# Kernel tuning notes

Hardware: AMD Instinct MI355X
Metric: run time of the kernel (lower is better)

The kernel has to match this reference:

```python
import jax, jax.numpy as jnp
import numpy as np

B, S, D, H, DFF = 2, 4096, 512, 8, 2048
DK = D // H
EPS = 1e-5


def layer_norm(x, g, b):
    mu = jnp.mean(x, axis=-1, keepdims=True)
    var = jnp.mean((x - mu) ** 2, axis=-1, keepdims=True)
    return (x - mu) * jax.lax.rsqrt(var + EPS) * g + b


def setup_inputs() -> dict:
    key = jax.random.key(0)
    ks = jax.random.split(key, 12)
    s = 1.0 / np.sqrt(D)
    return {
        "x": jax.random.normal(ks[0], (B, S, D), jnp.float32),
        "mask": jnp.ones((B, 1, 1, S), jnp.int32),
        "wq": jax.random.normal(ks[1], (D, D), jnp.float32) * s,
        "wk": jax.random.normal(ks[2], (D, D), jnp.float32) * s,
        "wv": jax.random.normal(ks[3], (D, D), jnp.float32) * s,
        "wo": jax.random.normal(ks[4], (D, D), jnp.float32) * s,
        "w1": jax.random.normal(ks[5], (D, DFF), jnp.float32) * s,
        "b1": jnp.zeros((DFF,), jnp.float32),
        "w2": jax.random.normal(ks[6], (DFF, D), jnp.float32) * (1.0 / np.sqrt(DFF)),
        "b2": jnp.zeros((D,), jnp.float32),
        "g1": jnp.ones((D,), jnp.float32),
        "be1": jnp.zeros((D,), jnp.float32),
        "g2": jnp.ones((D,), jnp.float32),
        "be2": jnp.zeros((D,), jnp.float32),
    }


def reference(x, mask, wq, wk, wv, wo, w1, b1, w2, b2, g1, be1, g2, be2):
    # projections -> [B, H, S, DK]
    def split_heads(t):
        return t.reshape(B, S, H, DK).transpose(0, 2, 1, 3)

    q = split_heads(x @ wq)
    k = split_heads(x @ wk)
    v = split_heads(x @ wv)

    scores = jnp.einsum("bhqd,bhkd->bhqk", q, k) / np.sqrt(DK)
    scores = jnp.where(mask == 0, -1e9, scores)
    attn = jax.nn.softmax(scores, axis=-1)  # dropout=0 (eval)
    ctx = jnp.einsum("bhqk,bhkd->bhqd", attn, v)
    ctx = ctx.transpose(0, 2, 1, 3).reshape(B, S, D)
    attn_out = ctx @ wo

    x1 = layer_norm(x + attn_out, g1, be1)
    ff = jax.nn.relu(x1 @ w1 + b1) @ w2 + b2
    return layer_norm(x1 + ff, g2, be2)
```

## Files before the change

kernel.cpp:

```cpp
#include <hip/hip_runtime.h>
#include <hip/hip_bf16.h>


typedef unsigned short u16;
typedef unsigned int u32;
typedef __attribute__((ext_vector_type(2))) u32 u32x2;
typedef __attribute__((ext_vector_type(4))) u16 u16x4;
typedef __attribute__((ext_vector_type(8))) u16 u16x8;
typedef __attribute__((ext_vector_type(2))) float f32x2;
typedef __attribute__((ext_vector_type(4))) float f32x4;
typedef __attribute__((ext_vector_type(16))) float f32x16;
typedef __attribute__((ext_vector_type(8))) short bf16x8;

#define CB 2
#define CS 4096
#define CD 512
#define CH 8
#define CDK 64
#define CDFF 2048
#define NXC ((size_t)CB * CS * CD)
#define NSP 2
#define BH (CB * CH)
#define BHS (BH * CS)

__device__ __forceinline__ float bf2f(u16 u) {
    union { u32 i; float f; } c;
    c.i = ((u32)u) << 16;
    return c.f;
}

__device__ __forceinline__ u16 f2bf(float f) {
    u32 x = __float_as_uint(f);
    u32 r = (x + 0x7fffu + ((x >> 16) & 1u)) >> 16;
    return (u16)r;
}

__device__ __forceinline__ u32 packbf2(float a, float b) {
    __hip_bfloat162 h = __float22bfloat162_rn(float2{a, b});
    union { __hip_bfloat162 h; u32 u; } c;
    c.h = h;
    return c.u;
}

__device__ __forceinline__ void dma16(const u16* g, u16* l) {
    __builtin_amdgcn_global_load_lds(
        (const __attribute__((address_space(1))) void*)g,
        (__attribute__((address_space(3))) void*)l, 16, 0, 0);
}

__global__ void detect_dtype(const u32* __restrict__ xw, int* __restrict__ flag) {
    __shared__ int red[256];
    int sane = 0;
    for (int i = threadIdx.x; i < 2048; i += 256) {
        u32 w = xw[i];
        u32 lo = w & 0xFFFFu;
        u32 e = (lo >> 7) & 0xFFu;
        if (lo == 0u || lo == 0x8000u || (e >= 96u && e <= 159u)) sane++;
    }
    red[threadIdx.x] = sane;
    __syncthreads();
    for (int s = 128; s > 0; s >>= 1) {
        if ((int)threadIdx.x < s) red[threadIdx.x] += red[threadIdx.x + s];
        __syncthreads();
    }
    if (threadIdx.x == 0) *flag = (red[0] >= 1843) ? 1 : 0;
}

__global__ __launch_bounds__(256) void convert_bf16(
    const void* __restrict__ src, u16* __restrict__ dst, int n,
    const int* __restrict__ flag)
{
    const bool isbf = (*flag != 0);
    const int n8 = n >> 3;
    int i = blockIdx.x * 256 + threadIdx.x;
    const int stride = gridDim.x * 256;
    if (isbf) {
        const u16x8* s = (const u16x8*)src;
        u16x8* d = (u16x8*)dst;
        for (; i < n8; i += stride) d[i] = s[i];
    } else {
        const f32x4* s = (const f32x4*)src;
        for (; i < n8; i += stride) {
            f32x4 a = s[2 * i];
            f32x4 b = s[2 * i + 1];
            u16x8 o;
#pragma unroll
            for (int e = 0; e < 4; e++) {
                o[e] = f2bf(a[e]);
                o[4 + e] = f2bf(b[e]);
            }
            *(u16x8*)&dst[(size_t)i * 8] = o;
        }
    }
    if (blockIdx.x == 0 && threadIdx.x == 0) {
        for (int r = n8 * 8; r < n; r++) {
            if (isbf) dst[r] = ((const u16*)src)[r];
            else dst[r] = f2bf(((const float*)src)[r]);
        }
    }
}

struct PrepArgs {
    const void* tsrc[6];
    u16* tdst[6];
    int R[6], Cc[6], nbx[6];
    int cum[7];
    const int* mask;
    unsigned long long* bits;
    const void* ssrc[6];
    u16* sdst[6];
    int sn[6];
};

__global__ __launch_bounds__(256) void prep_all(PrepArgs pa, const int* __restrict__ flag) {
    const int bid = blockIdx.x;
    const int tid = threadIdx.x;
    if (bid < pa.cum[6]) {
        __shared__ float t[32][33];
        int w = 0;
#pragma unroll
        for (int k = 1; k < 6; k++) w += (bid >= pa.cum[k]) ? 1 : 0;
        const int local = bid - pa.cum[w];
        const int nbx = pa.nbx[w];
        const int bx = local % nbx;
        const int by = local / nbx;
        const int R = pa.R[w];
        const int Cc = pa.Cc[w];
        const void* src = pa.tsrc[w];
        u16* dst = pa.tdst[w];
        const bool isbf = (*flag != 0);
        const int r0 = by * 32;
        const int c0 = bx * 32;
        const int col = tid & 31;
        const int row = tid >> 5;
#pragma unroll
        for (int it = 0; it < 4; it++) {
            int rr = row + it * 8;
            float v;
            if (isbf) v = bf2f(((const u16*)src)[(size_t)(r0 + rr) * Cc + c0 + col]);
            else v = ((const float*)src)[(size_t)(r0 + rr) * Cc + c0 + col];
            t[rr][col] = v;
        }
        __syncthreads();
#pragma unroll
        for (int it = 0; it < 4; it++) {
            int rr = row + it * 8;
            dst[(size_t)(c0 + rr) * R + r0 + col] = f2bf(t[col][rr]);
        }
    } else if (bid < pa.cum[6] + 32) {
        const int local = bid - pa.cum[6];
        int w = local * 4 + (tid >> 6);
        int lane = tid & 63;
        int b = w >> 6, t = w & 63;
        int val = pa.mask[b * CS + t * 64 + lane];
        unsigned long long bal = __ballot(val != 0);
        if (lane == 0) pa.bits[w] = bal;
    } else {
        const bool isbf = (*flag != 0);
        for (int t = 0; t < 6; t++) {
            for (int i = tid; i < pa.sn[t]; i += 256) {
                if (isbf) pa.sdst[t][i] = ((const u16*)pa.ssrc[t])[i];
                else pa.sdst[t][i] = f2bf(((const float*)pa.ssrc[t])[i]);
            }
        }
    }
}

#define F_SPLIT 1
#define F_BIAS  2
#define F_RELU  4

template <int FLAGS>
__global__ __launch_bounds__(512, 2) void gemm256(
    const u16* __restrict__ A, const u16* __restrict__ Bt,
    const u16* __restrict__ bias, u16* __restrict__ C,
    int M, int N, int K)
{
    __shared__ __align__(16) u16 POOL[65536 + 8 * 1536];

    const int tid = threadIdx.x;
    const int lane = tid & 63;
    const int wave = tid >> 6;
    const int lrow = lane & 15;
    const int quad = lane >> 4;
    const int rswg = lrow & 7;
    const int wm = wave >> 2;
    const int wn = wave & 3;
    const int m0 = blockIdx.y * 256;
    const int n0 = blockIdx.x * 256;

    const u16* Asrc[4];
    const u16* Bsrc[4];
#pragma unroll
    for (int r = 0; r < 4; r++) {
        const int idx = r * 512 + tid;
        const int row = idx >> 3;
        const int g = (idx & 7) ^ (row & 7);
        Asrc[r] = A + (size_t)(m0 + row) * K + g * 8;
        Bsrc[r] = Bt + (size_t)(n0 + row) * K + g * 8;
    }

#define STG256(BUF, K0)                                                      \
    {                                                                        \
        _Pragma("unroll")                                                    \
        for (int r = 0; r < 4; r++) {                                        \
            dma16(Asrc[r] + (K0), &POOL[(BUF) * 32768 + r * 4096 + wave * 512]); \
            dma16(Bsrc[r] + (K0), &POOL[(BUF) * 32768 + 16384 + r * 4096 + wave * 512]); \
        }                                                                    \
    }

    f32x4 acc[8][4];
#pragma unroll
    for (int mi = 0; mi < 8; mi++)
#pragma unroll
        for (int ni = 0; ni < 4; ni++) acc[mi][ni] = f32x4{0.f, 0.f, 0.f, 0.f};

    const int NT = K >> 6;
    STG256(0, 0)

    for (int j = 0; j < NT; j++) {
        asm volatile("s_waitcnt vmcnt(0)" ::: "memory");
        __builtin_amdgcn_sched_barrier(0);
        __builtin_amdgcn_s_barrier();
        __builtin_amdgcn_sched_barrier(0);
        if (j + 1 < NT) STG256((j + 1) & 1, (j + 1) * 64)

        const char* Ab = (const char*)&POOL[(j & 1) * 32768];
        const char* Bb = (const char*)&POOL[(j & 1) * 32768 + 16384];
#pragma unroll
        for (int ks = 0; ks < 2; ks++) {
            bf16x8 af[8], bfr[4];
#pragma unroll
            for (int mi = 0; mi < 8; mi++) {
                const int row = wm * 128 + mi * 16 + lrow;
                af[mi] = *(const bf16x8*)(Ab + row * 128 +
                                          (((ks * 4 + quad) ^ rswg) << 4));
            }
#pragma unroll
            for (int ni = 0; ni < 4; ni++) {
                const int row = wn * 64 + ni * 16 + lrow;
                bfr[ni] = *(const bf16x8*)(Bb + row * 128 +
                                           (((ks * 4 + quad) ^ rswg) << 4));
            }
#pragma unroll
            for (int mi = 0; mi < 8; mi++)
#pragma unroll
                for (int ni = 0; ni < 4; ni++)
                    acc[mi][ni] = __builtin_amdgcn_mfma_f32_16x16x32_bf16(
                        af[mi], bfr[ni], acc[mi][ni], 0, 0, 0);
        }
    }
#undef STG256

    u16* st = POOL + 65536 + wave * 1536;
    const int mbase = m0 + wm * 128;
    const int nbase = n0 + wn * 64;
    const int msub = mbase & 4095;
    const int bb = mbase >> 12;
    const bool vpath = (FLAGS & F_SPLIT) && ((nbase >> 9) == 2);

    if (vpath) {
        const int h = (nbase >> 6) & 7;
        u16* vdst = C + 2 * NXC + (((size_t)(bb * CH + h)) * CDK) * CS;
#pragma unroll
        for (int mi = 0; mi < 8; mi++) {
#pragma unroll
            for (int ni = 0; ni < 4; ni++)
#pragma unroll
                for (int r = 0; r < 4; r++)
                    st[(ni * 16 + lrow) * 24 + quad * 4 + r] = f2bf(acc[mi][ni][r]);
#pragma unroll
            for (int rr = 0; rr < 2; rr++) {
                const int idx = rr * 64 + lane;
                const int dk = idx >> 1;
                const int sch = idx & 1;
                u16x8 val = *(const u16x8*)&st[dk * 24 + sch * 8];
                *(u16x8*)&vdst[(size_t)dk * CS + msub + mi * 16 + sch * 8] = val;
            }
        }
    } else {
        float bv[4];
        if (FLAGS & F_BIAS) {
#pragma unroll
            for (int ni = 0; ni < 4; ni++) bv[ni] = bf2f(bias[nbase + ni * 16 + lrow]);
        }
        const int proj = nbase >> 9;
        const int h = (nbase >> 6) & 7;
        u16* qkdst = C + (size_t)proj * NXC + (((size_t)(bb * CH + h)) * CS) * CDK;
#pragma unroll
        for (int mi = 0; mi < 8; mi++) {
#pragma unroll
            for (int ni = 0; ni < 4; ni++)
#pragma unroll
                for (int r = 0; r < 4; r++) {
                    float val = acc[mi][ni][r];
                    if (FLAGS & F_BIAS) val += bv[ni];
                    if (FLAGS & F_RELU) val = fmaxf(val, 0.f);
                    st[(quad * 4 + r) * 68 + ni * 16 + lrow] = f2bf(val);
                }
#pragma unroll
            for (int rr = 0; rr < 2; rr++) {
                const int idx = rr * 64 + lane;
                const int row = idx >> 3;
                const int ch = idx & 7;
                u16x4 lo = *(const u16x4*)&st[row * 68 + ch * 8];
                u16x4 hi = *(const u16x4*)&st[row * 68 + ch * 8 + 4];
                u16x8 val;
#pragma unroll
                for (int e = 0; e < 4; e++) { val[e] = lo[e]; val[4 + e] = hi[e]; }
                u16* p;
                if (FLAGS & F_SPLIT)
                    p = qkdst + (size_t)(msub + mi * 16 + row) * CDK + ch * 8;
                else
                    p = C + (size_t)(mbase + mi * 16 + row) * N + nbase + ch * 8;
                *(u16x8*)p = val;
            }
        }
    }
}

template <int FLAGS, int PIPE>
__global__ __launch_bounds__(256, PIPE ? 1 : 3) void gemm_mfma(
    const u16* __restrict__ A, const u16* __restrict__ Bt,
    const u16* __restrict__ bias, u16* __restrict__ C,
    int M, int N, int K)
{
    constexpr int ABn = PIPE ? 12288 : 8192;
    __shared__ __align__(16) u16 POOL[2 * ABn + 4 * 1536];
    u16* ASb = POOL;
    u16* BSb = POOL + ABn;

    const int tid = threadIdx.x;
    const int lane = tid & 63;
    const int wave = tid >> 6;
    const int lrow = lane & 15;
    const int quad = lane >> 4;
    const int wm = wave & 1;
    const int wn = wave >> 1;
    const int m0 = blockIdx.y * 128;
    const int n0 = blockIdx.x * 128;

    f32x4 acc[4][4];
#pragma unroll
    for (int i = 0; i < 4; i++)
#pragma unroll
        for (int j = 0; j < 4; j++) acc[i][j] = f32x4{0.f, 0.f, 0.f, 0.f};

    if constexpr (PIPE) {
        const int idx0 = wave * 128 + lane;
        const int idx1 = idx0 + 64;
        const u16* Ap0 = A + (size_t)(m0 + (idx0 >> 2)) * K + (idx0 & 3) * 8;
        const u16* Ap1 = A + (size_t)(m0 + (idx1 >> 2)) * K + (idx1 & 3) * 8;
        const u16* Bp0 = Bt + (size_t)(n0 + (idx0 >> 2)) * K + (idx0 & 3) * 8;
        const u16* Bp1 = Bt + (size_t)(n0 + (idx1 >> 2)) * K + (idx1 & 3) * 8;
        const int NK = K >> 5;

#define PSTAGE(BOFF, KOFF)                                                   \
        {                                                                    \
            dma16(Ap0 + (KOFF), ASb + (BOFF) + wave * 1024);                 \
            dma16(Ap1 + (KOFF), ASb + (BOFF) + wave * 1024 + 512);           \
            dma16(Bp0 + (KOFF), BSb + (BOFF) + wave * 1024);                 \
            dma16(Bp1 + (KOFF), BSb + (BOFF) + wave * 1024 + 512);           \
        }
        PSTAGE(0, 0)
        PSTAGE(4096, 32)
        u32 bR = 0;
        for (int j = 0; j < NK; j++) {
            if (j < NK - 1) { asm volatile("s_waitcnt vmcnt(4)" ::: "memory"); }
            else            { asm volatile("s_waitcnt vmcnt(0)" ::: "memory"); }
            __builtin_amdgcn_sched_barrier(0);
            __builtin_amdgcn_s_barrier();
            __builtin_amdgcn_sched_barrier(0);
            if (j + 2 < NK) {
                u32 bS = bR + 8192;
                if (bS >= 12288) bS -= 12288;
                PSTAGE(bS, (j + 2) * 32)
            }
            bf16x8 af[4], bfr[4];
#pragma unroll
            for (int i = 0; i < 4; i++)
                af[i] = *(const bf16x8*)&ASb[bR + (wm * 64 + i * 16 + lrow) * 32 + quad * 8];
#pragma unroll
            for (int jj = 0; jj < 4; jj++)
                bfr[jj] = *(const bf16x8*)&BSb[bR + (wn * 64 + jj * 16 + lrow) * 32 + quad * 8];
#pragma unroll
            for (int i = 0; i < 4; i++)
#pragma unroll
                for (int jj = 0; jj < 4; jj++)
                    acc[i][jj] = __builtin_amdgcn_mfma_f32_16x16x32_bf16(
                        af[i], bfr[jj], acc[i][jj], 0, 0, 0);
            bR = (bR == 8192u) ? 0u : bR + 4096u;
        }
#undef PSTAGE
    } else {
        const int rswg = lrow & 7;
        const u16* Aps[4];
        const u16* Bps[4];
        u16* Adst[4];
        u16* Bdst[4];
#pragma unroll
        for (int r = 0; r < 4; r++) {
            const int idx = r * 256 + tid;
            const int row = idx >> 3;
            const int g = (idx & 7) ^ (row & 7);
            Aps[r] = A + (size_t)(m0 + row) * K + g * 8;
            Bps[r] = Bt + (size_t)(n0 + row) * K + g * 8;
            Adst[r] = &ASb[r * 2048 + wave * 512];
            Bdst[r] = &BSb[r * 2048 + wave * 512];
        }
        const char* As8 = (const char*)ASb;
        const char* Bs8 = (const char*)BSb;

        for (int k0 = 0; k0 < K; k0 += 64) {
            __syncthreads();
#pragma unroll
            for (int r = 0; r < 4; r++) {
                dma16(Aps[r] + k0, Adst[r]);
                dma16(Bps[r] + k0, Bdst[r]);
            }
            __syncthreads();

#pragma unroll
            for (int kk = 0; kk < 2; kk++) {
                bf16x8 af[4], bfr[4];
#pragma unroll
                for (int i = 0; i < 4; i++) {
                    const int row = wm * 64 + i * 16 + lrow;
                    af[i] = *(const bf16x8*)(As8 + row * 128 +
                                             (((kk * 4 + quad) ^ rswg) << 4));
                }
#pragma unroll
                for (int j = 0; j < 4; j++) {
                    const int row = wn * 64 + j * 16 + lrow;
                    bfr[j] = *(const bf16x8*)(Bs8 + row * 128 +
                                              (((kk * 4 + quad) ^ rswg) << 4));
                }
#pragma unroll
                for (int i = 0; i < 4; i++)
#pragma unroll
                    for (int j = 0; j < 4; j++)
                        acc[i][j] = __builtin_amdgcn_mfma_f32_16x16x32_bf16(
                            af[i], bfr[j], acc[i][j], 0, 0, 0);
            }
        }
    }

    u16* st = POOL + 2 * ABn + wave * 1536;
    const int mbase = m0 + wm * 64;
    const int nbase = n0 + wn * 64;
    const int msub = mbase & 4095;
    const int bb = mbase >> 12;
    const bool vpath = (FLAGS & F_SPLIT) && ((nbase >> 9) == 2);

    if (vpath) {
        const int h = (nbase >> 6) & 7;
        u16* vdst = C + 2 * NXC + (((size_t)(bb * CH + h)) * CDK) * CS;
#pragma unroll
        for (int i = 0; i < 4; i++) {
#pragma unroll
            for (int j = 0; j < 4; j++)
#pragma unroll
                for (int r = 0; r < 4; r++)
                    st[(j * 16 + lrow) * 24 + quad * 4 + r] = f2bf(acc[i][j][r]);
#pragma unroll
            for (int rr = 0; rr < 2; rr++) {
                const int idx = rr * 64 + lane;
                const int dk = idx >> 1;
                const int sch = idx & 1;
                u16x8 val = *(const u16x8*)&st[dk * 24 + sch * 8];
                *(u16x8*)&vdst[(size_t)dk * CS + msub + i * 16 + sch * 8] = val;
            }
        }
    } else {
        float bv[4];
        if (FLAGS & F_BIAS) {
#pragma unroll
            for (int j = 0; j < 4; j++) bv[j] = bf2f(bias[nbase + j * 16 + lrow]);
        }
        const int proj = nbase >> 9;
        const int h = (nbase >> 6) & 7;
        u16* qkdst = C + (size_t)proj * NXC + (((size_t)(bb * CH + h)) * CS) * CDK;
#pragma unroll
        for (int i = 0; i < 4; i++) {
#pragma unroll
            for (int j = 0; j < 4; j++)
#pragma unroll
                for (int r = 0; r < 4; r++) {
                    float val = acc[i][j][r];
                    if (FLAGS & F_BIAS) val += bv[j];
                    if (FLAGS & F_RELU) val = fmaxf(val, 0.f);
                    st[(quad * 4 + r) * 68 + j * 16 + lrow] = f2bf(val);
                }
#pragma unroll
            for (int rr = 0; rr < 2; rr++) {
                const int idx = rr * 64 + lane;
                const int row = idx >> 3;
                const int ch = idx & 7;
                u16x4 lo = *(const u16x4*)&st[row * 68 + ch * 8];
                u16x4 hi = *(const u16x4*)&st[row * 68 + ch * 8 + 4];
                u16x8 val;
#pragma unroll
                for (int e = 0; e < 4; e++) { val[e] = lo[e]; val[4 + e] = hi[e]; }
                u16* p;
                if (FLAGS & F_SPLIT)
                    p = qkdst + (size_t)(msub + i * 16 + row) * CDK + ch * 8;
                else
                    p = C + (size_t)(mbase + i * 16 + row) * N + nbase + ch * 8;
                *(u16x8*)p = val;
            }
        }
    }
}

__global__ __launch_bounds__(256, 4) void mfma_attn2(
    const u16* __restrict__ Qb, const u16* __restrict__ Kb,
    const u16* __restrict__ Vt, const unsigned long long* __restrict__ bits,
    u16* __restrict__ pOT, float* __restrict__ Ls)
{
    __shared__ u16 KB[3][4096];
    __shared__ u16 VB[2][4096];

    const int tid = threadIdx.x;
    const int lane = tid & 63;
    const int wave = tid >> 6;
    const int qcol = lane & 31;
    const int hf = lane >> 5;

    const int bh = blockIdx.y;
    const int b = bh >> 3;
    const int z = blockIdx.z;
    const int q0 = blockIdx.x * 128 + wave * 32;

    const float SC = 0.125f * 1.44269504088896340736f;

    bf16x8 bq[4];
    const u16* qp = Qb + ((size_t)bh * CS + q0 + qcol) * CDK + hf * 8;
#pragma unroll
    for (int c = 0; c < 4; c++) {
        bf16x8 raw = *(const bf16x8*)(qp + c * 16);
        union { u32 u[4]; bf16x8 v; } cv;
#pragma unroll
        for (int j = 0; j < 4; j++)
            cv.u[j] = packbf2(bf2f((u16)raw[2 * j]) * SC, bf2f((u16)raw[2 * j + 1]) * SC);
        bq[c] = cv.v;
    }

    f32x4 z4 = {0.f, 0.f, 0.f, 0.f};
    asm volatile("" : "+v"(z4));
    f32x16 zero16;
#pragma unroll
    for (int i = 0; i < 16; i++) zero16[i] = z4[i & 3];

    f32x16 ot[2];
#pragma unroll
    for (int dt = 0; dt < 2; dt++)
#pragma unroll
        for (int i = 0; i < 16; i++) ot[dt][i] = 0.f;
    float lh = 0.f;

    const u16* kbase = Kb + (size_t)bh * CS * CDK;
    const u16* vbase = Vt + (size_t)bh * CDK * CS;
    const unsigned long long* bp = bits + b * 64;

    const int t0 = z * (CS / NSP);
    const int t1 = t0 + (CS / NSP);

    const int rsw = qcol & 7;
    int koff[2][4];
#pragma unroll
    for (int rt = 0; rt < 2; rt++)
#pragma unroll
        for (int c = 0; c < 4; c++)
            koff[rt][c] = ((rt * 32 + qcol) * 64 + (((2 * c + hf) ^ rsw) * 8)) * 2;
    const char* kb0 = (const char*)&KB[0][0];
    const char* vb0 = (const char*)&VB[0][0];

    const int w2 = wave * 2;

#define STAGE_K(KOFFB, t)                                                    \
    {                                                                        \
        const u16* kb_ = kbase + (size_t)(t) * CDK;                          \
        _Pragma("unroll")                                                    \
        for (int n = 0; n < 2; n++) {                                        \
            int idx = (w2 + n) * 64 + lane;                                  \
            int row = idx >> 3;                                              \
            int g = (idx & 7) ^ (row & 7);                                   \
            dma16(kb_ + row * CDK + g * 8,                                   \
                  (u16*)((char*)&KB[0][0] + (KOFFB) + (w2 + n) * 1024));     \
        }                                                                    \
    }
#define STAGE_V(P, t)                                                        \
    {                                                                        \
        const u16* vb_ = vbase + (t);                                        \
        _Pragma("unroll")                                                    \
        for (int n = 0; n < 2; n++) {                                        \
            int idx = (w2 + n) * 64 + lane;                                  \
            int row = idx >> 3;                                              \
            int g = (idx & 7) ^ (row & 7);                                   \
            dma16(vb_ + (size_t)row * CS + g * 8,                            \
                  (u16*)((char*)&VB[0][0] + (P) * 8192 + (w2 + n) * 1024));  \
        }                                                                    \
    }

#define TBODY(KROFF, VOFF, BM, MASKED, MIDSYNC)                              \
    {                                                                        \
        f32x2 racc = {0.f, 0.f};                                             \
        _Pragma("unroll")                                                    \
        for (int mt = 0; mt < 2; mt++) {                                     \
            f32x16 s;                                                        \
            _Pragma("unroll")                                                \
            for (int c = 0; c < 4; c++) {                                    \
                bf16x8 ak = *(const bf16x8*)(kb0 + (KROFF) + koff[mt][c]);   \
                s = __builtin_amdgcn_mfma_f32_32x32x16_bf16(                 \
                    ak, bq[c], (c == 0) ? zero16 : s, 0, 0, 0);              \
            }                                                                \
            if (MASKED) {                                                    \
                const unsigned long long bm_ = (BM);                         \
                if (bm_ != ~0ull) {                                          \
                    _Pragma("unroll")                                        \
                    for (int i = 0; i < 16; i++) {                           \
                        const int key = (i & 3) + 8 * (i >> 2) + 4 * hf + 32 * mt; \
                        if (!((bm_ >> key) & 1ull)) s[i] = -1e30f;           \
                    }                                                        \
                }                                                            \
            }                                                                \
            u32 pk[8];                                                       \
            _Pragma("unroll")                                                \
            for (int g = 0; g < 4; g++) {                                    \
                float p0 = __builtin_amdgcn_exp2f(s[4 * g + 0]);             \
                float p1 = __builtin_amdgcn_exp2f(s[4 * g + 1]);             \
                float p2 = __builtin_amdgcn_exp2f(s[4 * g + 2]);             \
                float p3 = __builtin_amdgcn_exp2f(s[4 * g + 3]);             \
                racc += f32x2{p0, p1};                                       \
                racc += f32x2{p2, p3};                                       \
                pk[2 * g + 0] = packbf2(p0, p1);                             \
                pk[2 * g + 1] = packbf2(p2, p3);                             \
            }                                                                \
            if (mt == 0) { MIDSYNC }                                         \
            _Pragma("unroll")                                                \
            for (int cc = 0; cc < 2; cc++) {                                 \
                u32x2 r0 = __builtin_amdgcn_permlane32_swap(                 \
                    pk[4 * cc + 0], pk[4 * cc + 2], false, false);           \
                u32x2 r1 = __builtin_amdgcn_permlane32_swap(                 \
                    pk[4 * cc + 1], pk[4 * cc + 3], false, false);           \
                union { u32 u[4]; bf16x8 v; } pf;                            \
                pf.u[0] = r0.x;                                              \
                pf.u[1] = r1.x;                                              \
                pf.u[2] = r0.y;                                              \
                pf.u[3] = r1.y;                                              \
                const int c = 2 * mt + cc;                                   \
                _Pragma("unroll")                                            \
                for (int dt = 0; dt < 2; dt++) {                             \
                    bf16x8 av = *(const bf16x8*)(vb0 + (VOFF) + koff[dt][c]); \
                    ot[dt] = __builtin_amdgcn_mfma_f32_32x32x16_bf16(        \
                        av, pf.v, ot[dt], 0, 0, 0);                          \
                }                                                            \
            }                                                                \
        }                                                                    \
        lh += racc.x + racc.y;                                               \
    }

#define FTILE(P, TT, KR, KS, DOV, DOK, TOPASM, MIDASM)                       \
    {                                                                        \
        asm volatile(TOPASM ::: "memory");                                   \
        __builtin_amdgcn_sched_barrier(0);                                   \
        __builtin_amdgcn_s_barrier();                                        \
        __builtin_amdgcn_sched_barrier(0);                                   \
        if (DOV) STAGE_V((P) ^ 1, (TT) + 64);                                \
        if (DOK) STAGE_K((KS), (TT) + 128);                                  \
        TBODY((KR), (P) * 8192, 0ull, 0,                                     \
              asm volatile(MIDASM ::: "memory");                             \
              __builtin_amdgcn_sched_barrier(0);                             \
              __builtin_amdgcn_s_barrier();                                  \
              __builtin_amdgcn_sched_barrier(0);)                            \
    }

    unsigned long long am = ~0ull;
    const int tb0 = t0 >> 6;
    for (int i = 0; i < 32; i++) am &= bp[tb0 + i];
    const bool allones = (am == ~0ull);

    if (allones) {
        STAGE_K(0, t0);
        STAGE_V(0, t0);
        STAGE_K(8192, t0 + 64);

        u32 kr = 0;
        for (int m = 0; m < 15; m++) {
            const int t = t0 + m * 128;
            const u32 kr1 = (kr == 16384u) ? 0u : kr + 8192u;
            const u32 ks0 = (kr1 == 16384u) ? 0u : kr1 + 8192u;
            FTILE(0, t, kr, ks0, 1, 1,
                  "s_waitcnt vmcnt(4)", "s_waitcnt vmcnt(6)")
            FTILE(1, t + 64, kr1, kr, 1, 1,
                  "s_waitcnt vmcnt(4)", "s_waitcnt vmcnt(6)")
            kr = ks0;
        }
        {
            const int t = t0 + 30 * 64;
            const u32 kr1 = (kr == 16384u) ? 0u : kr + 8192u;
            FTILE(0, t, kr, 0, 1, 0,
                  "s_waitcnt vmcnt(4)", "s_waitcnt vmcnt(4)")
            FTILE(1, t + 64, kr1, 0, 0, 0,
                  "s_waitcnt vmcnt(2)", "s_waitcnt vmcnt(0)")
        }
    } else {
        STAGE_K(0, t0);
        STAGE_V(0, t0);
        __syncthreads();
        for (int t = t0; t < t1; t += 64) {
            const int p = (t >> 6) & 1;
            const u32 kro = (u32)p * 8192u;
            if (t + 64 < t1) {
                STAGE_V(p ^ 1, t + 64);
                STAGE_K((p ^ 1) * 8192, t + 64);
            }
            TBODY(kro, p * 8192, bp[t >> 6], 1, ;)
            __syncthreads();
        }
    }
#undef FTILE
#undef TBODY
#undef STAGE_V
#undef STAGE_K

    u32x2 rr = __builtin_amdgcn_permlane32_swap(
        __float_as_uint(lh), __float_as_uint(lh), false, false);
    const float l = lh + __uint_as_float(hf ? rr.x : rr.y);

    const int q_lin = bh * CS + q0 + qcol;
    if (hf == 0) Ls[z * BHS + q_lin] = l;
    const size_t pbase = ((size_t)(z * BH + bh) * CDK) * CS + q0 + qcol;
#pragma unroll
    for (int dt = 0; dt < 2; dt++)
#pragma unroll
        for (int i = 0; i < 16; i++) {
            const int dk = (i & 3) + 8 * (i >> 2) + 4 * hf + 32 * dt;
            pOT[pbase + (size_t)dk * CS] = f2bf(ot[dt][i]);
        }
}

__global__ __launch_bounds__(256) void attn_combine(
    const u16* __restrict__ pOT, const float* __restrict__ Ls,
    u16* __restrict__ ctx)
{
    __shared__ float linv[64];
    __shared__ u16 T[64][72];

    const int bh = blockIdx.y;
    const int s0 = blockIdx.x * 64;
    const int b = bh >> 3, h = bh & 7;
    const int tid = threadIdx.x;

    if (tid < 64) {
        float L = 0.f;
#pragma unroll
        for (int z = 0; z < NSP; z++) L += Ls[z * BHS + bh * CS + s0 + tid];
        linv[tid] = (L > 0.f) ? 1.f / L : 0.f;
    }
    __syncthreads();

    const int dk = tid >> 2;
    const int sc = (tid & 3) * 16;
    float acc[16] = {};
#pragma unroll
    for (int z = 0; z < NSP; z++) {
        const u16* p = pOT + ((size_t)(z * BH + bh) * CDK + dk) * CS + s0 + sc;
        u16x8 v0 = *(const u16x8*)p;
        u16x8 v1 = *(const u16x8*)(p + 8);
#pragma unroll
        for (int e = 0; e < 8; e++) {
            acc[e] += bf2f(v0[e]);
            acc[8 + e] += bf2f(v1[e]);
        }
    }
#pragma unroll
    for (int e = 0; e < 16; e++)
        T[sc + e][dk] = f2bf(acc[e] * linv[sc + e]);
    __syncthreads();

    const int sr = tid >> 2;
    const int dc = (tid & 3) * 16;
    u16x8 o0, o1;
#pragma unroll
    for (int e = 0; e < 8; e++) {
        o0[e] = T[sr][dc + e];
        o1[e] = T[sr][dc + 8 + e];
    }
    u16* cp = &ctx[((size_t)b * CS + s0 + sr) * CD + h * CDK + dc];
    *(u16x8*)cp = o0;
    *(u16x8*)(cp + 8) = o1;
}

__global__ __launch_bounds__(256) void ln_kernel(
    const u16* __restrict__ xa, const u16* __restrict__ xb,
    const u16* __restrict__ g, const u16* __restrict__ be,
    u16* __restrict__ outb, float* __restrict__ outf,
    const int* __restrict__ flag)
{
    const int lane = threadIdx.x & 63;
    const int wave = threadIdx.x >> 6;
    const size_t row = (size_t)blockIdx.x * 4 + wave;
    const int c0 = lane * 8;

    u16x8 av = *(const u16x8*)(xa + row * CD + c0);
    u16x8 bv = *(const u16x8*)(xb + row * CD + c0);

    float v[8];
    float s1 = 0.f, s2 = 0.f;
#pragma unroll
    for (int e = 0; e < 8; e++) {
        v[e] = bf2f(av[e]) + bf2f(bv[e]);
        s1 += v[e];
        s2 += v[e] * v[e];
    }
#pragma unroll
    for (int off = 32; off > 0; off >>= 1) {
        s1 += __shfl_xor(s1, off, 64);
        s2 += __shfl_xor(s2, off, 64);
    }
    const float mu = s1 * (1.f / CD);
    const float var = fmaxf(s2 * (1.f / CD) - mu * mu, 0.f);
    const float r = rsqrtf(var + 1e-5f);

    u16x8 gv = *(const u16x8*)(g + c0);
    u16x8 ev = *(const u16x8*)(be + c0);
    float res[8];
#pragma unroll
    for (int e = 0; e < 8; e++)
        res[e] = (v[e] - mu) * r * bf2f(gv[e]) + bf2f(ev[e]);

    const int flg = *flag;
    const bool f32out = (outf != nullptr) && (flg == 0);
    if (f32out) {
        float4 o0 = make_float4(res[0], res[1], res[2], res[3]);
        float4 o1 = make_float4(res[4], res[5], res[6], res[7]);
        *(float4*)(outf + row * CD + c0) = o0;
        *(float4*)(outf + row * CD + c0 + 4) = o1;
    } else {
        u16x8 ov;
#pragma unroll
        for (int e = 0; e < 8; e++) ov[e] = f2bf(res[e]);
        *(u16x8*)(outb + row * CD + c0) = ov;
    }
}


extern "C" void kernel_launch(void* const* d_in, const int* in_sizes, int n_in,
                              void* d_out, int out_size, void* d_ws, size_t ws_size,
                              hipStream_t stream)
{
    const void* x_raw   = d_in[0];
    const int*  mask    = (const int*)d_in[1];
    const void* wq_raw  = d_in[2];
    const void* wk_raw  = d_in[3];
    const void* wv_raw  = d_in[4];
    const void* wo_raw  = d_in[5];
    const void* w1_raw  = d_in[6];
    const void* b1_raw  = d_in[7];
    const void* w2_raw  = d_in[8];
    const void* b2_raw  = d_in[9];
    const void* g1_raw  = d_in[10];
    const void* be1_raw = d_in[11];
    const void* g2_raw  = d_in[12];
    const void* be2_raw = d_in[13];

    const size_t NX = NXC;
    const size_t WSZ = (size_t)CD * CD;
    const size_t W1SZ = (size_t)CD * CDFF;

    u16* ws = (u16*)d_ws;
    int* flag = (int*)d_ws;
    unsigned long long* bits = (unsigned long long*)(ws + 512);
    u16* base = ws + 1024;
    u16* xc  = base;
    u16* q   = base + 1 * NX;
    u16* k   = base + 2 * NX;
    u16* v   = base + 3 * NX;
    u16* ctx = base + 4 * NX;
    u16* att = base + 5 * NX;
    u16* x1  = base + 6 * NX;
    u16* ffo = base + 7 * NX;
    u16* ffh = base + 8 * NX;
    u16* wt  = base + 12 * NX;
    u16* wqkvT = wt;
    u16* woT = wqkvT + 3 * WSZ;
    u16* w1T = woT + WSZ;
    u16* w2T = w1T + W1SZ;
    u16* b1c = w2T + W1SZ;
    u16* b2c = b1c + CDFF;
    u16* g1c = b2c + CD;
    u16* be1c = g1c + CD;
    u16* g2c = be1c + CD;
    u16* be2c = g2c + CD;
    u16* wend = be2c + CD;

    const size_t need = (size_t)(wend - ws) * sizeof(u16);
    if (ws_size < need) return;
    (void)k;

    u16* pOT = ffh;
    float* Ls = (float*)att;

    detect_dtype<<<1, 256, 0, stream>>>((const u32*)x_raw, flag);

    convert_bf16<<<1024, 256, 0, stream>>>(x_raw, xc, (int)NX, flag);

    PrepArgs pa;
    pa.tsrc[0] = wq_raw; pa.tdst[0] = wqkvT;           pa.R[0] = CD;   pa.Cc[0] = CD;
    pa.tsrc[1] = wk_raw; pa.tdst[1] = wqkvT + WSZ;     pa.R[1] = CD;   pa.Cc[1] = CD;
    pa.tsrc[2] = wv_raw; pa.tdst[2] = wqkvT + 2 * WSZ; pa.R[2] = CD;   pa.Cc[2] = CD;
    pa.tsrc[3] = wo_raw; pa.tdst[3] = woT;             pa.R[3] = CD;   pa.Cc[3] = CD;
    pa.tsrc[4] = w1_raw; pa.tdst[4] = w1T;             pa.R[4] = CD;   pa.Cc[4] = CDFF;
    pa.tsrc[5] = w2_raw; pa.tdst[5] = w2T;             pa.R[5] = CDFF; pa.Cc[5] = CD;
    int cum = 0;
    for (int w = 0; w < 6; w++) {
        pa.nbx[w] = pa.Cc[w] / 32;
        pa.cum[w] = cum;
        cum += (pa.Cc[w] / 32) * (pa.R[w] / 32);
    }
    pa.cum[6] = cum;
    pa.mask = mask;
    pa.bits = bits;
    pa.ssrc[0] = b1_raw;  pa.sdst[0] = b1c;  pa.sn[0] = CDFF;
    pa.ssrc[1] = b2_raw;  pa.sdst[1] = b2c;  pa.sn[1] = CD;
    pa.ssrc[2] = g1_raw;  pa.sdst[2] = g1c;  pa.sn[2] = CD;
    pa.ssrc[3] = be1_raw; pa.sdst[3] = be1c; pa.sn[3] = CD;
    pa.ssrc[4] = g2_raw;  pa.sdst[4] = g2c;  pa.sn[4] = CD;
    pa.ssrc[5] = be2_raw; pa.sdst[5] = be2c; pa.sn[5] = CD;
    prep_all<<<cum + 32 + 1, 256, 0, stream>>>(pa, flag);

    const int M = CB * CS;

    gemm256<F_SPLIT><<<dim3(1536 / 256, M / 256), 512, 0, stream>>>(
        xc, wqkvT, nullptr, q, M, 1536, CD);

    mfma_attn2<<<dim3(CS / 128, BH, NSP), 256, 0, stream>>>(q, k, v, bits, pOT, Ls);
    attn_combine<<<dim3(CS / 64, BH), 256, 0, stream>>>(pOT, Ls, ctx);

    gemm_mfma<0, 1><<<dim3(CD / 128, M / 128), 256, 0, stream>>>(
        ctx, woT, nullptr, att, M, CD, CD);

    ln_kernel<<<dim3(M / 4), 256, 0, stream>>>(xc, att, g1c, be1c, x1, nullptr, flag);

    gemm256<F_BIAS | F_RELU><<<dim3(CDFF / 256, M / 256), 512, 0, stream>>>(
        x1, w1T, b1c, ffh, M, CDFF, CD);
    gemm_mfma<F_BIAS, 1><<<dim3(CD / 128, M / 128), 256, 0, stream>>>(
        ffh, w2T, b2c, ffo, M, CD, CDFF);

    ln_kernel<<<dim3(M / 4), 256, 0, stream>>>(x1, ffo, g2c, be2c,
                                               (u16*)d_out, (float*)d_out, flag);
}
```

Baseline: 300.9 us.

## Deepen GEMM prefetch pipeline, remap attention blocks per XCD, prioritize MFMA

The PIPE GEMM goes from a 3-slot to a 6-slot LDS ring buffer, keeping five stages of global-to-LDS DMA in flight with an explicitly drained tail to hide more memory latency. The attention launch becomes a flat 1D grid whose block index is decoded so each XCD handles contiguous (bh, split) pairs, aiming for better L2 reuse of K/V. s_setprio is raised around the attention MFMA sequences to favour issue of matrix work. The larger GEMM LDS footprint may reduce occupancy, though that kernel already runs one block per SM.

```diff
diff --git a/kernel.cpp b/kernel.cpp
--- a/kernel.cpp
+++ b/kernel.cpp
@@ -325,7 +325,7 @@
     const u16* __restrict__ bias, u16* __restrict__ C,
     int M, int N, int K)
 {
-    constexpr int ABn = PIPE ? 12288 : 8192;
+    constexpr int ABn = PIPE ? 24576 : 8192;
     __shared__ __align__(16) u16 POOL[2 * ABn + 4 * 1536];
     u16* ASb = POOL;
     u16* BSb = POOL + ABn;
@@ -362,35 +362,48 @@
             dma16(Bp0 + (KOFF), BSb + (BOFF) + wave * 1024);                 \
             dma16(Bp1 + (KOFF), BSb + (BOFF) + wave * 1024 + 512);           \
         }
+#define PITER(VMASM, DOS, JS)                                                \
+        {                                                                    \
+            asm volatile(VMASM ::: "memory");                                \
+            __builtin_amdgcn_sched_barrier(0);                               \
+            __builtin_amdgcn_s_barrier();                                    \
+            __builtin_amdgcn_sched_barrier(0);                               \
+            if (DOS) {                                                       \
+                u32 bS = bR + 20480u;                                        \
+                if (bS >= 24576u) bS -= 24576u;                              \
+                PSTAGE(bS, ((JS) + 5) * 32)                                  \
+            }                                                                \
+            bf16x8 af[4], bfr[4];                                            \
+            _Pragma("unroll")                                                \
+            for (int i = 0; i < 4; i++)                                      \
+                af[i] = *(const bf16x8*)&ASb[bR + (wm * 64 + i * 16 + lrow) * 32 + quad * 8]; \
+            _Pragma("unroll")                                                \
+            for (int jj = 0; jj < 4; jj++)                                   \
+                bfr[jj] = *(const bf16x8*)&BSb[bR + (wn * 64 + jj * 16 + lrow) * 32 + quad * 8]; \
+            _Pragma("unroll")                                                \
+            for (int i = 0; i < 4; i++)                                      \
+                _Pragma("unroll")                                            \
+                for (int jj = 0; jj < 4; jj++)                               \
+                    acc[i][jj] = __builtin_amdgcn_mfma_f32_16x16x32_bf16(    \
+                        af[i], bfr[jj], acc[i][jj], 0, 0, 0);                \
+            bR += 4096u;                                                     \
+            if (bR == 24576u) bR = 0u;                                       \
+        }
+
         PSTAGE(0, 0)
         PSTAGE(4096, 32)
+        PSTAGE(8192, 64)
+        PSTAGE(12288, 96)
+        PSTAGE(16384, 128)
         u32 bR = 0;
-        for (int j = 0; j < NK; j++) {
-            if (j < NK - 1) { asm volatile("s_waitcnt vmcnt(4)" ::: "memory"); }
-            else            { asm volatile("s_waitcnt vmcnt(0)" ::: "memory"); }
-            __builtin_amdgcn_sched_barrier(0);
-            __builtin_amdgcn_s_barrier();
-            __builtin_amdgcn_sched_barrier(0);
-            if (j + 2 < NK) {
-                u32 bS = bR + 8192;
-                if (bS >= 12288) bS -= 12288;
-                PSTAGE(bS, (j + 2) * 32)
-            }
-            bf16x8 af[4], bfr[4];
-#pragma unroll
-            for (int i = 0; i < 4; i++)
-                af[i] = *(const bf16x8*)&ASb[bR + (wm * 64 + i * 16 + lrow) * 32 + quad * 8];
-#pragma unroll
-            for (int jj = 0; jj < 4; jj++)
-                bfr[jj] = *(const bf16x8*)&BSb[bR + (wn * 64 + jj * 16 + lrow) * 32 + quad * 8];
-#pragma unroll
-            for (int i = 0; i < 4; i++)
-#pragma unroll
-                for (int jj = 0; jj < 4; jj++)
-                    acc[i][jj] = __builtin_amdgcn_mfma_f32_16x16x32_bf16(
-                        af[i], bfr[jj], acc[i][jj], 0, 0, 0);
-            bR = (bR == 8192u) ? 0u : bR + 4096u;
-        }
+        for (int js = 0; js < NK - 4; js++) {
+            PITER("s_waitcnt vmcnt(16)", (js + 5 < NK), js)
+        }
+        PITER("s_waitcnt vmcnt(12)", 0, 0)
+        PITER("s_waitcnt vmcnt(8)", 0, 0)
+        PITER("s_waitcnt vmcnt(4)", 0, 0)
+        PITER("s_waitcnt vmcnt(0)", 0, 0)
+#undef PITER
 #undef PSTAGE
     } else {
         const int rswg = lrow & 7;
@@ -526,10 +539,15 @@
     const int qcol = lane & 31;
     const int hf = lane >> 5;
 
-    const int bh = blockIdx.y;
+    const int id = blockIdx.x;
+    const int xcd = id & 7;
+    const int jL = id >> 3;
+    const int p = ((jL >> 5) << 3) | xcd;
+    const int qx = jL & 31;
+    const int bh = p >> 1;
+    const int z = p & 1;
     const int b = bh >> 3;
-    const int z = blockIdx.z;
-    const int q0 = blockIdx.x * 128 + wave * 32;
+    const int q0 = qx * 128 + wave * 32;
 
     const float SC = 0.125f * 1.44269504088896340736f;
 
@@ -608,12 +626,14 @@
         _Pragma("unroll")                                                    \
         for (int mt = 0; mt < 2; mt++) {                                     \
             f32x16 s;                                                        \
+            __builtin_amdgcn_s_setprio(1);                                   \
             _Pragma("unroll")                                                \
             for (int c = 0; c < 4; c++) {                                    \
                 bf16x8 ak = *(const bf16x8*)(kb0 + (KROFF) + koff[mt][c]);   \
                 s = __builtin_amdgcn_mfma_f32_32x32x16_bf16(                 \
                     ak, bq[c], (c == 0) ? zero16 : s, 0, 0, 0);              \
             }                                                                \
+            __builtin_amdgcn_s_setprio(0);                                   \
             if (MASKED) {                                                    \
                 const unsigned long long bm_ = (BM);                         \
                 if (bm_ != ~0ull) {                                          \
@@ -649,12 +669,14 @@
                 pf.u[2] = r0.y;                                              \
                 pf.u[3] = r1.y;                                              \
                 const int c = 2 * mt + cc;                                   \
+                __builtin_amdgcn_s_setprio(1);                               \
                 _Pragma("unroll")                                            \
                 for (int dt = 0; dt < 2; dt++) {                             \
                     bf16x8 av = *(const bf16x8*)(vb0 + (VOFF) + koff[dt][c]); \
                     ot[dt] = __builtin_amdgcn_mfma_f32_32x32x16_bf16(        \
                         av, pf.v, ot[dt], 0, 0, 0);                          \
                 }                                                            \
+                __builtin_amdgcn_s_setprio(0);                               \
             }                                                                \
         }                                                                    \
         lh += racc.x + racc.y;                                               \
@@ -709,13 +731,13 @@
         STAGE_V(0, t0);
         __syncthreads();
         for (int t = t0; t < t1; t += 64) {
-            const int p = (t >> 6) & 1;
-            const u32 kro = (u32)p * 8192u;
+            const int pp = (t >> 6) & 1;
+            const u32 kro = (u32)pp * 8192u;
             if (t + 64 < t1) {
-                STAGE_V(p ^ 1, t + 64);
-                STAGE_K((p ^ 1) * 8192, t + 64);
-            }
-            TBODY(kro, p * 8192, bp[t >> 6], 1, ;)
+                STAGE_V(pp ^ 1, t + 64);
+                STAGE_K((pp ^ 1) * 8192, t + 64);
+            }
+            TBODY(kro, pp * 8192, bp[t >> 6], 1, ;)
             __syncthreads();
         }
     }
@@ -935,7 +957,7 @@
     gemm256<F_SPLIT><<<dim3(1536 / 256, M / 256), 512, 0, stream>>>(
         xc, wqkvT, nullptr, q, M, 1536, CD);
 
-    mfma_attn2<<<dim3(CS / 128, BH, NSP), 256, 0, stream>>>(q, k, v, bits, pOT, Ls);
+    mfma_attn2<<<dim3(1024), 256, 0, stream>>>(q, k, v, bits, pOT, Ls);
     attn_combine<<<dim3(CS / 64, BH), 256, 0, stream>>>(pOT, Ls, ctx);
 
     gemm_mfma<0, 1><<<dim3(CD / 128, M / 128), 256, 0, stream>>>(
```

After: 302.3 us. About the same (+0.5%).

## Fold dtype detection and x conversion into prep, remap grids for XCD locality

Applied to the files above, without the earlier changes.

Removes the separate detect_dtype and convert_bf16 launches. Every prep_all block now recomputes the dtype check itself, and 1024 extra blocks in prep_all convert x. The gemm256 and attention kernels switch to a 1D grid with a block-id remap intended to place related tiles on the same XCD for better L2 reuse. It also adds s_setprio around the MFMA sequences in attention. The trade-off is redundant dtype-detection reads in every prep block.

```diff
diff --git a/kernel.cpp b/kernel.cpp
--- a/kernel.cpp
+++ b/kernel.cpp
@@ -48,58 +48,6 @@
         (__attribute__((address_space(3))) void*)l, 16, 0, 0);
 }
 
-__global__ void detect_dtype(const u32* __restrict__ xw, int* __restrict__ flag) {
-    __shared__ int red[256];
-    int sane = 0;
-    for (int i = threadIdx.x; i < 2048; i += 256) {
-        u32 w = xw[i];
-        u32 lo = w & 0xFFFFu;
-        u32 e = (lo >> 7) & 0xFFu;
-        if (lo == 0u || lo == 0x8000u || (e >= 96u && e <= 159u)) sane++;
-    }
-    red[threadIdx.x] = sane;
-    __syncthreads();
-    for (int s = 128; s > 0; s >>= 1) {
-        if ((int)threadIdx.x < s) red[threadIdx.x] += red[threadIdx.x + s];
-        __syncthreads();
-    }
-    if (threadIdx.x == 0) *flag = (red[0] >= 1843) ? 1 : 0;
-}
-
-__global__ __launch_bounds__(256) void convert_bf16(
-    const void* __restrict__ src, u16* __restrict__ dst, int n,
-    const int* __restrict__ flag)
-{
-    const bool isbf = (*flag != 0);
-    const int n8 = n >> 3;
-    int i = blockIdx.x * 256 + threadIdx.x;
-    const int stride = gridDim.x * 256;
-    if (isbf) {
-        const u16x8* s = (const u16x8*)src;
-        u16x8* d = (u16x8*)dst;
-        for (; i < n8; i += stride) d[i] = s[i];
-    } else {
-        const f32x4* s = (const f32x4*)src;
-        for (; i < n8; i += stride) {
-            f32x4 a = s[2 * i];
-            f32x4 b = s[2 * i + 1];
-            u16x8 o;
-#pragma unroll
-            for (int e = 0; e < 4; e++) {
-                o[e] = f2bf(a[e]);
-                o[4 + e] = f2bf(b[e]);
-            }
-            *(u16x8*)&dst[(size_t)i * 8] = o;
-        }
-    }
-    if (blockIdx.x == 0 && threadIdx.x == 0) {
-        for (int r = n8 * 8; r < n; r++) {
-            if (isbf) dst[r] = ((const u16*)src)[r];
-            else dst[r] = f2bf(((const float*)src)[r]);
-        }
-    }
-}
-
 struct PrepArgs {
     const void* tsrc[6];
     u16* tdst[6];
@@ -110,13 +58,35 @@
     const void* ssrc[6];
     u16* sdst[6];
     int sn[6];
+    const u32* xw;
+    const void* xsrc;
+    u16* xdst;
+    int xn8;
 };
 
-__global__ __launch_bounds__(256) void prep_all(PrepArgs pa, const int* __restrict__ flag) {
+__global__ __launch_bounds__(256) void prep_all(PrepArgs pa, int* __restrict__ flag) {
+    __shared__ int red[256];
+    __shared__ float t[32][33];
     const int bid = blockIdx.x;
     const int tid = threadIdx.x;
+
+    int sane = 0;
+    for (int i = tid; i < 2048; i += 256) {
+        u32 w = pa.xw[i];
+        u32 lo = w & 0xFFFFu;
+        u32 e = (lo >> 7) & 0xFFu;
+        if (lo == 0u || lo == 0x8000u || (e >= 96u && e <= 159u)) sane++;
+    }
+    red[tid] = sane;
+    __syncthreads();
+    for (int s = 128; s > 0; s >>= 1) {
+        if (tid < s) red[tid] += red[tid + s];
+        __syncthreads();
+    }
+    const bool isbf = (red[0] >= 1843);
+    if (bid == 0 && tid == 0) *flag = isbf ? 1 : 0;
+
     if (bid < pa.cum[6]) {
-        __shared__ float t[32][33];
         int w = 0;
 #pragma unroll
         for (int k = 1; k < 6; k++) w += (bid >= pa.cum[k]) ? 1 : 0;
@@ -128,7 +98,6 @@
         const int Cc = pa.Cc[w];
         const void* src = pa.tsrc[w];
         u16* dst = pa.tdst[w];
-        const bool isbf = (*flag != 0);
         const int r0 = by * 32;
         const int c0 = bx * 32;
         const int col = tid & 31;
@@ -151,16 +120,37 @@
         const int local = bid - pa.cum[6];
         int w = local * 4 + (tid >> 6);
         int lane = tid & 63;
-        int b = w >> 6, t = w & 63;
-        int val = pa.mask[b * CS + t * 64 + lane];
+        int b = w >> 6, tt = w & 63;
+        int val = pa.mask[b * CS + tt * 64 + lane];
         unsigned long long bal = __ballot(val != 0);
         if (lane == 0) pa.bits[w] = bal;
+    } else if (bid == pa.cum[6] + 32) {
+        for (int tc = 0; tc < 6; tc++) {
+            for (int i = tid; i < pa.sn[tc]; i += 256) {
+                if (isbf) pa.sdst[tc][i] = ((const u16*)pa.ssrc[tc])[i];
+                else pa.sdst[tc][i] = f2bf(((const float*)pa.ssrc[tc])[i]);
+            }
+        }
     } else {
-        const bool isbf = (*flag != 0);
-        for (int t = 0; t < 6; t++) {
-            for (int i = tid; i < pa.sn[t]; i += 256) {
-                if (isbf) pa.sdst[t][i] = ((const u16*)pa.ssrc[t])[i];
-                else pa.sdst[t][i] = f2bf(((const float*)pa.ssrc[t])[i]);
+        const int local = bid - (pa.cum[6] + 33);
+        int i = local * 256 + tid;
+        const int stride = 1024 * 256;
+        if (isbf) {
+            const u16x8* s = (const u16x8*)pa.xsrc;
+            u16x8* d = (u16x8*)pa.xdst;
+            for (; i < pa.xn8; i += stride) d[i] = s[i];
+        } else {
+            const f32x4* s = (const f32x4*)pa.xsrc;
+            for (; i < pa.xn8; i += stride) {
+                f32x4 a = s[2 * i];
+                f32x4 b = s[2 * i + 1];
+                u16x8 o;
+#pragma unroll
+                for (int e = 0; e < 4; e++) {
+                    o[e] = f2bf(a[e]);
+                    o[4 + e] = f2bf(b[e]);
+                }
+                *(u16x8*)&pa.xdst[(size_t)i * 8] = o;
             }
         }
     }
@@ -186,8 +176,16 @@
     const int rswg = lrow & 7;
     const int wm = wave >> 2;
     const int wn = wave & 3;
-    const int m0 = blockIdx.y * 256;
-    const int n0 = blockIdx.x * 256;
+
+    const int id = blockIdx.x;
+    const int nx = N >> 8;
+    const int p = id & 7;
+    const int q = id >> 3;
+    const int qd = q / nx;
+    const int by = p * 4 + qd;
+    const int bx = q - qd * nx;
+    const int m0 = by * 256;
+    const int n0 = bx * 256;
 
     const u16* Asrc[4];
     const u16* Bsrc[4];
@@ -308,12 +306,12 @@
                 u16x8 val;
 #pragma unroll
                 for (int e = 0; e < 4; e++) { val[e] = lo[e]; val[4 + e] = hi[e]; }
-                u16* p;
+                u16* pp;
                 if (FLAGS & F_SPLIT)
-                    p = qkdst + (size_t)(msub + mi * 16 + row) * CDK + ch * 8;
+                    pp = qkdst + (size_t)(msub + mi * 16 + row) * CDK + ch * 8;
                 else
-                    p = C + (size_t)(mbase + mi * 16 + row) * N + nbase + ch * 8;
-                *(u16x8*)p = val;
+                    pp = C + (size_t)(mbase + mi * 16 + row) * N + nbase + ch * 8;
+                *(u16x8*)pp = val;
             }
         }
     }
@@ -501,12 +499,12 @@
                 u16x8 val;
 #pragma unroll
                 for (int e = 0; e < 4; e++) { val[e] = lo[e]; val[4 + e] = hi[e]; }
-                u16* p;
+                u16* pp;
                 if (FLAGS & F_SPLIT)
-                    p = qkdst + (size_t)(msub + i * 16 + row) * CDK + ch * 8;
+                    pp = qkdst + (size_t)(msub + i * 16 + row) * CDK + ch * 8;
                 else
-                    p = C + (size_t)(mbase + i * 16 + row) * N + nbase + ch * 8;
-                *(u16x8*)p = val;
+                    pp = C + (size_t)(mbase + i * 16 + row) * N + nbase + ch * 8;
+                *(u16x8*)pp = val;
             }
         }
     }
@@ -526,10 +524,15 @@
     const int qcol = lane & 31;
     const int hf = lane >> 5;
 
-    const int bh = blockIdx.y;
+    const int id = blockIdx.x;
+    const int xcd = id & 7;
+    const int jL = id >> 3;
+    const int p = ((jL >> 5) << 3) | xcd;
+    const int qx = jL & 31;
+    const int bh = p >> 1;
+    const int z = p & 1;
     const int b = bh >> 3;
-    const int z = blockIdx.z;
-    const int q0 = blockIdx.x * 128 + wave * 32;
+    const int q0 = qx * 128 + wave * 32;
 
     const float SC = 0.125f * 1.44269504088896340736f;
 
@@ -608,12 +611,14 @@
         _Pragma("unroll")                                                    \
         for (int mt = 0; mt < 2; mt++) {                                     \
             f32x16 s;                                                        \
+            __builtin_amdgcn_s_setprio(1);                                   \
             _Pragma("unroll")                                                \
             for (int c = 0; c < 4; c++) {                                    \
                 bf16x8 ak = *(const bf16x8*)(kb0 + (KROFF) + koff[mt][c]);   \
                 s = __builtin_amdgcn_mfma_f32_32x32x16_bf16(                 \
                     ak, bq[c], (c == 0) ? zero16 : s, 0, 0, 0);              \
             }                                                                \
+            __builtin_amdgcn_s_setprio(0);                                   \
             if (MASKED) {                                                    \
                 const unsigned long long bm_ = (BM);                         \
                 if (bm_ != ~0ull) {                                          \
@@ -649,12 +654,14 @@
                 pf.u[2] = r0.y;                                              \
                 pf.u[3] = r1.y;                                              \
                 const int c = 2 * mt + cc;                                   \
+                __builtin_amdgcn_s_setprio(1);                               \
                 _Pragma("unroll")                                            \
                 for (int dt = 0; dt < 2; dt++) {                             \
                     bf16x8 av = *(const bf16x8*)(vb0 + (VOFF) + koff[dt][c]); \
                     ot[dt] = __builtin_amdgcn_mfma_f32_32x32x16_bf16(        \
                         av, pf.v, ot[dt], 0, 0, 0);                          \
                 }                                                            \
+                __builtin_amdgcn_s_setprio(0);                               \
             }                                                                \
         }                                                                    \
         lh += racc.x + racc.y;                                               \
@@ -709,13 +716,13 @@
         STAGE_V(0, t0);
         __syncthreads();
         for (int t = t0; t < t1; t += 64) {
-            const int p = (t >> 6) & 1;
-            const u32 kro = (u32)p * 8192u;
+            const int pp = (t >> 6) & 1;
+            const u32 kro = (u32)pp * 8192u;
             if (t + 64 < t1) {
-                STAGE_V(p ^ 1, t + 64);
-                STAGE_K((p ^ 1) * 8192, t + 64);
-            }
-            TBODY(kro, p * 8192, bp[t >> 6], 1, ;)
+                STAGE_V(pp ^ 1, t + 64);
+                STAGE_K((pp ^ 1) * 8192, t + 64);
+            }
+            TBODY(kro, pp * 8192, bp[t >> 6], 1, ;)
             __syncthreads();
         }
     }
@@ -902,10 +909,6 @@
     u16* pOT = ffh;
     float* Ls = (float*)att;
 
-    detect_dtype<<<1, 256, 0, stream>>>((const u32*)x_raw, flag);
-
-    convert_bf16<<<1024, 256, 0, stream>>>(x_raw, xc, (int)NX, flag);
-
     PrepArgs pa;
     pa.tsrc[0] = wq_raw; pa.tdst[0] = wqkvT;           pa.R[0] = CD;   pa.Cc[0] = CD;
     pa.tsrc[1] = wk_raw; pa.tdst[1] = wqkvT + WSZ;     pa.R[1] = CD;   pa.Cc[1] = CD;
@@ -928,14 +931,18 @@
     pa.ssrc[3] = be1_raw; pa.sdst[3] = be1c; pa.sn[3] = CD;
     pa.ssrc[4] = g2_raw;  pa.sdst[4] = g2c;  pa.sn[4] = CD;
     pa.ssrc[5] = be2_raw; pa.sdst[5] = be2c; pa.sn[5] = CD;
-    prep_all<<<cum + 32 + 1, 256, 0, stream>>>(pa, flag);
+    pa.xw = (const u32*)x_raw;
+    pa.xsrc = x_raw;
+    pa.xdst = xc;
+    pa.xn8 = (int)(NX >> 3);
+    prep_all<<<cum + 32 + 1 + 1024, 256, 0, stream>>>(pa, flag);
 
     const int M = CB * CS;
 
-    gemm256<F_SPLIT><<<dim3(1536 / 256, M / 256), 512, 0, stream>>>(
+    gemm256<F_SPLIT><<<dim3((1536 / 256) * (M / 256)), 512, 0, stream>>>(
         xc, wqkvT, nullptr, q, M, 1536, CD);
 
-    mfma_attn2<<<dim3(CS / 128, BH, NSP), 256, 0, stream>>>(q, k, v, bits, pOT, Ls);
+    mfma_attn2<<<dim3(1024), 256, 0, stream>>>(q, k, v, bits, pOT, Ls);
     attn_combine<<<dim3(CS / 64, BH), 256, 0, stream>>>(pOT, Ls, ctx);
 
     gemm_mfma<0, 1><<<dim3(CD / 128, M / 128), 256, 0, stream>>>(
@@ -943,7 +950,7 @@
 
     ln_kernel<<<dim3(M / 4), 256, 0, stream>>>(xc, att, g1c, be1c, x1, nullptr, flag);
 
-    gemm256<F_BIAS | F_RELU><<<dim3(CDFF / 256, M / 256), 512, 0, stream>>>(
+    gemm256<F_BIAS | F_RELU><<<dim3((CDFF / 256) * (M / 256)), 512, 0, stream>>>(
         x1, w1T, b1c, ffh, M, CDFF, CD);
     gemm_mfma<F_BIAS, 1><<<dim3(CD / 128, M / 128), 256, 0, stream>>>(
         ffh, w2T, b2c, ffo, M, CD, CDFF);
```

Result: faster. 287.3 us (-4.5%).
